# Performance work log

Hardware: AMD Instinct MI355X
Metric: run time of the kernel (lower is better)

## Reference

```python
import jax, jax.numpy as jnp
import numpy as np

N = 8192
IN_F = 512
OUT_F = 512
ALPHA = 0.2  # leaky relu slope


def setup_inputs() -> dict:
    key = jax.random.key(0)
    k1, k2, k3, k4, k5 = jax.random.split(key, 5)
    inp = jax.random.normal(k1, (N, IN_F), dtype=jnp.float32)
    adj = jax.random.randint(k2, (N, N), 0, 2, dtype=jnp.int32)
    # linear1: [in, out] + bias
    W1 = jax.random.normal(k3, (IN_F, OUT_F), dtype=jnp.float32) * (1.0 / np.sqrt(IN_F))
    b1 = jnp.zeros((OUT_F,), dtype=jnp.float32)
    # linear2: maps 2*out -> 1; split into the two halves acting on h_i and h_j
    a = jax.random.normal(k4, (2 * OUT_F,), dtype=jnp.float32) * (1.0 / np.sqrt(2 * OUT_F))
    a1 = a[:OUT_F]
    a2 = a[OUT_F:]
    b2 = jnp.zeros((), dtype=jnp.float32)
    return {"inp": inp, "adj": adj, "W1": W1, "b1": b1, "a1": a1, "a2": a2, "b2": b2}


def reference(inp, adj, W1, b1, a1, a2, b2):
    h = inp @ W1 + b1  # [N, out]
    # linear2(cat(h_i, h_j)) == h_i@a1 + h_j@a2 + b2 -> avoids the N*N*2F tensor
    e = jax.nn.leaky_relu((h @ a1)[:, None] + (h @ a2)[None, :] + b2, ALPHA)  # [N, N]
    attention = jnp.where(adj > 0, e, jnp.float32(-1e12))
    attention = jax.nn.softmax(attention, axis=1)
    h_prime = attention @ h  # [N, out]
    return jax.nn.elu(h_prime)  # concat=True
```

## Files before the change

kernel.cpp:

```cpp
#include <hip/hip_runtime.h>
#include <hip/hip_bf16.h>
#include <stdint.h>

#define NR 8192
#define FD 512
#define BM 64
#define BKC 128

typedef __attribute__((ext_vector_type(8))) short s8v;
typedef __attribute__((ext_vector_type(4))) float f32x4;

static __device__ __forceinline__ short bf16_rtne(float x) {
    union { float f; uint32_t u; } v; v.f = x;
    uint32_t r = (v.u + 0x7FFFu + ((v.u >> 16) & 1u)) >> 16;
    return (short)r;
}
static __device__ __forceinline__ float bf16_to_f32(short s) {
    union { uint32_t u; float f; } v; v.u = ((uint32_t)(uint16_t)s) << 16;
    return v.f;
}

__global__ void k_prepack(const int* __restrict__ adj, uint32_t* __restrict__ bm) {
    int t = blockIdx.x * 256 + threadIdx.x;
    const int4* p = (const int4*)(adj + (size_t)t * 32);
    uint32_t word = 0;
#pragma unroll
    for (int g = 0; g < 8; ++g) {
        int4 v = p[g];
        word |= (uint32_t)(v.x != 0) << (g * 4);
        word |= (uint32_t)(v.y != 0) << (g * 4 + 1);
        word |= (uint32_t)(v.z != 0) << (g * 4 + 2);
        word |= (uint32_t)(v.w != 0) << (g * 4 + 3);
    }
    bm[t] = word;
}

__global__ void k_convert(const float* __restrict__ in, short* __restrict__ out) {
    int i = blockIdx.x * blockDim.x + threadIdx.x;
    float4 v = ((const float4*)in)[i];
    short4 s;
    s.x = bf16_rtne(v.x); s.y = bf16_rtne(v.y);
    s.z = bf16_rtne(v.z); s.w = bf16_rtne(v.w);
    ((short4*)out)[i] = s;
}

__global__ void k_w1t(const float* __restrict__ W1, short* __restrict__ W1T) {
    int i = blockIdx.x * 256 + threadIdx.x;
    int k = i & 511, n = i >> 9;
    W1T[(size_t)n * 512 + k] = bf16_rtne(W1[(size_t)k * 512 + n]);
}

__launch_bounds__(256)
__global__ void k_gemm_h(const short* __restrict__ A,
                         const short* __restrict__ BT,
                         const float* __restrict__ b1,
                         short* __restrict__ H,
                         short* __restrict__ HT2)
{
    const int lane = threadIdx.x & 63;
    const int wn   = threadIdx.x >> 6;
    const int m    = lane & 15;
    const int q    = lane >> 4;
    const int r0   = blockIdx.x * 32;
    const int c0   = blockIdx.y * 128 + wn * 32;

    f32x4 acc[2][2] = {};
#pragma unroll 1
    for (int k0 = 0; k0 < 512; k0 += 32) {
        s8v a[2], b[2];
#pragma unroll
        for (int rt = 0; rt < 2; ++rt)
            a[rt] = *(const s8v*)(A + (size_t)(r0 + rt * 16 + m) * 512 + k0 + q * 8);
#pragma unroll
        for (int nt = 0; nt < 2; ++nt)
            b[nt] = *(const s8v*)(BT + (size_t)(c0 + nt * 16 + m) * 512 + k0 + q * 8);
#pragma unroll
        for (int rt = 0; rt < 2; ++rt)
#pragma unroll
            for (int nt = 0; nt < 2; ++nt)
                acc[rt][nt] = __builtin_amdgcn_mfma_f32_16x16x32_bf16(a[rt], b[nt], acc[rt][nt], 0, 0, 0);
    }
    float b1v[2];
#pragma unroll
    for (int nt = 0; nt < 2; ++nt) b1v[nt] = b1[c0 + nt * 16 + m];

#pragma unroll
    for (int rt = 0; rt < 2; ++rt)
#pragma unroll
        for (int nt = 0; nt < 2; ++nt) {
            int col = c0 + nt * 16 + m;
            short4 hp;
#pragma unroll
            for (int r = 0; r < 4; ++r) {
                int row = r0 + rt * 16 + q * 4 + r;
                short hv = bf16_rtne(acc[rt][nt][r] + b1v[nt]);
                H[(size_t)row * 512 + col] = hv;
                ((short*)&hp)[r] = hv;
            }
            *(short4*)(HT2 + (size_t)blockIdx.x * (512 * 32) + (size_t)col * 32 + rt * 16 + q * 4) = hp;
        }
}

__global__ void k_f1f2(const short* __restrict__ H, const float* __restrict__ a1,
                       const float* __restrict__ a2, const float* __restrict__ b2,
                       float* __restrict__ f1, float* __restrict__ f2s)
{
    const int lane = threadIdx.x & 63;
    const int row  = blockIdx.x * 4 + (threadIdx.x >> 6);
    s8v hv = *(const s8v*)(H + (size_t)row * 512 + lane * 8);
    float4 a1l = ((const float4*)(a1 + lane * 8))[0];
    float4 a1h = ((const float4*)(a1 + lane * 8))[1];
    float4 a2l = ((const float4*)(a2 + lane * 8))[0];
    float4 a2h = ((const float4*)(a2 + lane * 8))[1];
    float hf[8];
#pragma unroll
    for (int i = 0; i < 8; ++i) hf[i] = bf16_to_f32(hv[i]);
    float s1 = hf[0] * a1l.x + hf[1] * a1l.y + hf[2] * a1l.z + hf[3] * a1l.w
             + hf[4] * a1h.x + hf[5] * a1h.y + hf[6] * a1h.z + hf[7] * a1h.w;
    float s2 = hf[0] * a2l.x + hf[1] * a2l.y + hf[2] * a2l.z + hf[3] * a2l.w
             + hf[4] * a2h.x + hf[5] * a2h.y + hf[6] * a2h.z + hf[7] * a2h.w;
#pragma unroll
    for (int o = 32; o > 0; o >>= 1) {
        s1 += __shfl_xor(s1, o);
        s2 += __shfl_xor(s2, o);
    }
    if (lane == 0) {
        f1[row]  = s1;
        f2s[row] = s2 + b2[0];
    }
}

__launch_bounds__(512, 4)
__global__ void k_attn(const uint32_t* __restrict__ bm,
                       const short* __restrict__ HT2,
                       const float* __restrict__ f1,
                       const float* __restrict__ f2s,
                       float* __restrict__ nump,
                       float* __restrict__ denomp)
{
    __shared__ __align__(16) short wt[2][BM * BKC];

    const int t    = threadIdx.x;
    const int lane = t & 63;
    const int w    = t >> 6;
    const int m    = lane & 15;
    const int q    = lane >> 4;

    const int js   = blockIdx.x & 3;
    const int band = blockIdx.x >> 2;
    const int r0   = band * BM;
    const int jb0  = js * 2048;

    const int prow = t >> 3;
    const int jg   = t & 7;

    const float f1v = f1[r0 + prow];
    const uint16_t* bmp = (const uint16_t*)(bm + (size_t)(r0 + prow) * 256) + (jb0 >> 4) + jg;
    const float*    f2p = f2s + jb0 + jg * 16;

    f32x4 acc[4][4] = {};
    float dsum = 0.f;

    uint32_t bits = bmp[0];
    float4 fv[4];
#pragma unroll
    for (int g = 0; g < 4; ++g) fv[g] = ((const float4*)f2p)[g];

#pragma unroll 1
    for (int ch = 0; ch < 2048 / BKC; ++ch) {
        const int p = ch & 1;
        float wgt[16];
#pragma unroll
        for (int jj = 0; jj < 16; ++jj) {
            float s  = f1v + ((const float*)fv)[jj];
            float l  = fmaxf(s, 0.2f * s);
            float e  = __expf(l);
            float wv = ((bits >> jj) & 1u) ? e : 0.f;
            dsum += wv;
            wgt[jj] = wv;
        }
        s8v wv0, wv1;
#pragma unroll
        for (int jj = 0; jj < 8; ++jj) {
            wv0[jj] = bf16_rtne(wgt[jj]);
            wv1[jj] = bf16_rtne(wgt[8 + jj]);
        }
        const int sw = prow & 15;
        *(s8v*)&wt[p][prow * BKC + (((2 * jg) ^ sw) << 3)]     = wv0;
        *(s8v*)&wt[p][prow * BKC + (((2 * jg + 1) ^ sw) << 3)] = wv1;

        __syncthreads();

        const int chn = (ch + 1) & (2048 / BKC - 1);
        bits = bmp[chn * 8];
#pragma unroll
        for (int g = 0; g < 4; ++g) fv[g] = ((const float4*)(f2p + chn * BKC))[g];

#pragma unroll
        for (int kk = 0; kk < 4; ++kk) {
            const int jt = (jb0 + ch * BKC + kk * 32) >> 5;
            const short* hb = HT2 + (size_t)jt * 16384 + q * 8;
            s8v af[4];
#pragma unroll
            for (int i = 0; i < 4; ++i) {
                int row = i * 16 + m;
                af[i] = *(const s8v*)&wt[p][row * BKC + (((kk * 4 + q) ^ m) << 3)];
            }
#pragma unroll
            for (int nt = 0; nt < 4; ++nt) {
                s8v b = *(const s8v*)(hb + (size_t)(w * 64 + nt * 16 + m) * 32);
#pragma unroll
                for (int i = 0; i < 4; ++i)
                    acc[i][nt] = __builtin_amdgcn_mfma_f32_16x16x32_bf16(af[i], b, acc[i][nt], 0, 0, 0);
            }
        }
    }

    dsum += __shfl_xor(dsum, 1);
    dsum += __shfl_xor(dsum, 2);
    dsum += __shfl_xor(dsum, 4);
    if (jg == 0) denomp[(size_t)js * NR + r0 + prow] = dsum;

    float* np = nump + (size_t)js * NR * FD;
#pragma unroll
    for (int i = 0; i < 4; ++i)
#pragma unroll
        for (int nt = 0; nt < 4; ++nt)
#pragma unroll
            for (int r = 0; r < 4; ++r) {
                int row = r0 + i * 16 + q * 4 + r;
                int col = w * 64 + nt * 16 + m;
                np[(size_t)row * FD + col] = acc[i][nt][r];
            }
}

__global__ void k_combine(const float* __restrict__ nump,
                          const float* __restrict__ denomp,
                          float* __restrict__ out)
{
    size_t e = ((size_t)blockIdx.x * 256 + threadIdx.x) * 4;
    int row = (int)(e >> 9);
    float4 n0 = *(const float4*)(nump + e);
    float4 n1 = *(const float4*)(nump + (size_t)NR * FD + e);
    float4 n2 = *(const float4*)(nump + (size_t)2 * NR * FD + e);
    float4 n3 = *(const float4*)(nump + (size_t)3 * NR * FD + e);
    float d = denomp[row] + denomp[NR + row] + denomp[2 * NR + row] + denomp[3 * NR + row];
    float inv = 1.0f / d;
    float4 o;
    o.x = (n0.x + n1.x + n2.x + n3.x) * inv;
    o.y = (n0.y + n1.y + n2.y + n3.y) * inv;
    o.z = (n0.z + n1.z + n2.z + n3.z) * inv;
    o.w = (n0.w + n1.w + n2.w + n3.w) * inv;
    o.x = (o.x > 0.f) ? o.x : (__expf(o.x) - 1.f);
    o.y = (o.y > 0.f) ? o.y : (__expf(o.y) - 1.f);
    o.z = (o.z > 0.f) ? o.z : (__expf(o.z) - 1.f);
    o.w = (o.w > 0.f) ? o.w : (__expf(o.w) - 1.f);
    *(float4*)(out + e) = o;
}

extern "C" void kernel_launch(void* const* d_in, const int* in_sizes, int n_in,
                              void* d_out, int out_size, void* d_ws, size_t ws_size,
                              hipStream_t stream) {
    const float* inp = (const float*)d_in[0];
    const int*   adj = (const int*)d_in[1];
    const float* W1  = (const float*)d_in[2];
    const float* b1  = (const float*)d_in[3];
    const float* a1  = (const float*)d_in[4];
    const float* a2  = (const float*)d_in[5];
    const float* b2  = (const float*)d_in[6];
    float* out = (float*)d_out;

    short*    inp_bf = (short*)d_ws;
    short*    w1t    = inp_bf + (size_t)NR * FD;
    short*    h      = w1t + (size_t)FD * FD;
    short*    ht2    = h + (size_t)NR * FD;
    uint32_t* bmw    = (uint32_t*)(ht2 + (size_t)FD * NR);
    float*    f1     = (float*)(bmw + (size_t)NR * 256);
    float*    f2s    = f1 + NR;
    float*    nump   = f2s + NR;
    float*    denomp = nump + (size_t)4 * NR * FD;

    k_prepack<<<NR * 256 / 256, 256, 0, stream>>>(adj, bmw);
    k_convert<<<(NR * FD / 4) / 256, 256, 0, stream>>>(inp, inp_bf);
    k_w1t<<<(FD * FD) / 256, 256, 0, stream>>>(W1, w1t);
    dim3 g1(NR / 32, FD / 128);
    k_gemm_h<<<g1, 256, 0, stream>>>(inp_bf, w1t, b1, h, ht2);
    k_f1f2<<<NR / 4, 256, 0, stream>>>(h, a1, a2, b2, f1, f2s);
    k_attn<<<128 * 4, 512, 0, stream>>>(bmw, ht2, f1, f2s, nump, denomp);
    k_combine<<<(NR * FD / 4) / 256, 256, 0, stream>>>(nump, denomp, out);
}
```

Baseline: 565.9 us.

## Pipeline attention weight generation with MFMA, widen block, ballot-based adjacency packing

Restructures the attention kernel to use 1024-thread blocks with a 256-wide K chunk. The exp/mask weight computation for the next chunk now runs after the current chunk's MFMAs, so one barrier per iteration separates the LDS double buffer and the exp work can overlap matrix math. Each wave now covers 32 output columns instead of 64, which lowers accumulator register pressure but halves reuse of the A fragments. The adjacency prepack is rewritten to build 64-bit masks with wave ballots and fully coalesced int loads, changing the bit layout to match.

```diff
diff --git a/kernel.cpp b/kernel.cpp
--- a/kernel.cpp
+++ b/kernel.cpp
@@ -5,7 +5,7 @@
 #define NR 8192
 #define FD 512
 #define BM 64
-#define BKC 128
+#define BKC 256
 
 typedef __attribute__((ext_vector_type(8))) short s8v;
 typedef __attribute__((ext_vector_type(4))) float f32x4;
@@ -20,19 +20,25 @@
     return v.f;
 }
 
-__global__ void k_prepack(const int* __restrict__ adj, uint32_t* __restrict__ bm) {
-    int t = blockIdx.x * 256 + threadIdx.x;
-    const int4* p = (const int4*)(adj + (size_t)t * 32);
-    uint32_t word = 0;
+__global__ void k_prepack(const int* __restrict__ adj,
+                          unsigned long long* __restrict__ bm) {
+    const int lane = threadIdx.x & 63;
+    const int wv   = threadIdx.x >> 6;
+    const int gid  = blockIdx.x * 4 + wv;
+    const int row  = gid >> 2;
+    const int seg  = (gid & 3) * 2048;
+    const int* p   = adj + (size_t)row * NR + seg + lane;
+    unsigned long long* o = bm + (((size_t)row * NR + seg) >> 6);
 #pragma unroll
     for (int g = 0; g < 8; ++g) {
-        int4 v = p[g];
-        word |= (uint32_t)(v.x != 0) << (g * 4);
-        word |= (uint32_t)(v.y != 0) << (g * 4 + 1);
-        word |= (uint32_t)(v.z != 0) << (g * 4 + 2);
-        word |= (uint32_t)(v.w != 0) << (g * 4 + 3);
-    }
-    bm[t] = word;
+        unsigned long long b0 = __ballot(p[g * 256]       != 0);
+        unsigned long long b1 = __ballot(p[g * 256 + 64]  != 0);
+        unsigned long long b2 = __ballot(p[g * 256 + 128] != 0);
+        unsigned long long b3 = __ballot(p[g * 256 + 192] != 0);
+        unsigned long long vs = (lane == 0) ? b0 : (lane == 1) ? b1
+                              : (lane == 2) ? b2 : b3;
+        if (lane < 4) o[g * 4 + lane] = vs;
+    }
 }
 
 __global__ void k_convert(const float* __restrict__ in, short* __restrict__ out) {
@@ -130,7 +136,7 @@
     }
 }
 
-__launch_bounds__(512, 4)
+__launch_bounds__(1024, 4)
 __global__ void k_attn(const uint32_t* __restrict__ bm,
                        const short* __restrict__ HT2,
                        const float* __restrict__ f1,
@@ -151,85 +157,98 @@
     const int r0   = band * BM;
     const int jb0  = js * 2048;
 
-    const int prow = t >> 3;
-    const int jg   = t & 7;
+    const int prow = t >> 4;
+    const int jg   = t & 15;
 
     const float f1v = f1[r0 + prow];
-    const uint16_t* bmp = (const uint16_t*)(bm + (size_t)(r0 + prow) * 256) + (jb0 >> 4) + jg;
+    const uint16_t* bmp = (const uint16_t*)bm + (((size_t)(r0 + prow) * NR + jb0) >> 4) + jg;
     const float*    f2p = f2s + jb0 + jg * 16;
 
-    f32x4 acc[4][4] = {};
+    f32x4 acc[4][2] = {};
     float dsum = 0.f;
 
-    uint32_t bits = bmp[0];
+    uint32_t bits;
     float4 fv[4];
+
+#define GAT_PHASE1(PN)                                                        \
+    {                                                                         \
+        s8v wv0, wv1;                                                         \
+        _Pragma("unroll")                                                     \
+        for (int jj = 0; jj < 8; ++jj) {                                      \
+            float s_ = f1v + ((const float*)fv)[jj];                          \
+            float e_ = __expf(fmaxf(s_, 0.2f * s_));                          \
+            float x_ = ((bits >> jj) & 1u) ? e_ : 0.f;                        \
+            dsum += x_;                                                       \
+            wv0[jj] = bf16_rtne(x_);                                          \
+        }                                                                     \
+        _Pragma("unroll")                                                     \
+        for (int jj = 0; jj < 8; ++jj) {                                      \
+            float s_ = f1v + ((const float*)fv)[8 + jj];                      \
+            float e_ = __expf(fmaxf(s_, 0.2f * s_));                          \
+            float x_ = ((bits >> (8 + jj)) & 1u) ? e_ : 0.f;                  \
+            dsum += x_;                                                       \
+            wv1[jj] = bf16_rtne(x_);                                          \
+        }                                                                     \
+        const int sw = prow & 15;                                             \
+        *(s8v*)&wt[PN][prow * BKC + (((2 * jg) ^ sw) << 3)]     = wv0;        \
+        *(s8v*)&wt[PN][prow * BKC + (((2 * jg + 1) ^ sw) << 3)] = wv1;        \
+    }
+
+    bits = bmp[0];
 #pragma unroll
     for (int g = 0; g < 4; ++g) fv[g] = ((const float4*)f2p)[g];
+    GAT_PHASE1(0)
+    __syncthreads();
 
 #pragma unroll 1
     for (int ch = 0; ch < 2048 / BKC; ++ch) {
-        const int p = ch & 1;
-        float wgt[16];
-#pragma unroll
-        for (int jj = 0; jj < 16; ++jj) {
-            float s  = f1v + ((const float*)fv)[jj];
-            float l  = fmaxf(s, 0.2f * s);
-            float e  = __expf(l);
-            float wv = ((bits >> jj) & 1u) ? e : 0.f;
-            dsum += wv;
-            wgt[jj] = wv;
+        const int p   = ch & 1;
+        const int chn = ch + 1;
+        const bool more = (chn < 2048 / BKC);
+        if (more) {
+            bits = bmp[chn * 16];
+#pragma unroll
+            for (int g = 0; g < 4; ++g) fv[g] = ((const float4*)(f2p + chn * BKC))[g];
         }
-        s8v wv0, wv1;
-#pragma unroll
-        for (int jj = 0; jj < 8; ++jj) {
-            wv0[jj] = bf16_rtne(wgt[jj]);
-            wv1[jj] = bf16_rtne(wgt[8 + jj]);
-        }
-        const int sw = prow & 15;
-        *(s8v*)&wt[p][prow * BKC + (((2 * jg) ^ sw) << 3)]     = wv0;
-        *(s8v*)&wt[p][prow * BKC + (((2 * jg + 1) ^ sw) << 3)] = wv1;
-
-        __syncthreads();
-
-        const int chn = (ch + 1) & (2048 / BKC - 1);
-        bits = bmp[chn * 8];
-#pragma unroll
-        for (int g = 0; g < 4; ++g) fv[g] = ((const float4*)(f2p + chn * BKC))[g];
-
-#pragma unroll
-        for (int kk = 0; kk < 4; ++kk) {
+
+#pragma unroll
+        for (int kk = 0; kk < 8; ++kk) {
             const int jt = (jb0 + ch * BKC + kk * 32) >> 5;
             const short* hb = HT2 + (size_t)jt * 16384 + q * 8;
+            s8v b0 = *(const s8v*)(hb + (size_t)(w * 32 + m) * 32);
+            s8v b1 = *(const s8v*)(hb + (size_t)(w * 32 + 16 + m) * 32);
             s8v af[4];
 #pragma unroll
+            for (int i = 0; i < 4; ++i)
+                af[i] = *(const s8v*)&wt[p][(i * 16 + m) * BKC + (((kk * 4 + q) ^ m) << 3)];
+#pragma unroll
             for (int i = 0; i < 4; ++i) {
-                int row = i * 16 + m;
-                af[i] = *(const s8v*)&wt[p][row * BKC + (((kk * 4 + q) ^ m) << 3)];
-            }
-#pragma unroll
-            for (int nt = 0; nt < 4; ++nt) {
-                s8v b = *(const s8v*)(hb + (size_t)(w * 64 + nt * 16 + m) * 32);
-#pragma unroll
-                for (int i = 0; i < 4; ++i)
-                    acc[i][nt] = __builtin_amdgcn_mfma_f32_16x16x32_bf16(af[i], b, acc[i][nt], 0, 0, 0);
+                acc[i][0] = __builtin_amdgcn_mfma_f32_16x16x32_bf16(af[i], b0, acc[i][0], 0, 0, 0);
+                acc[i][1] = __builtin_amdgcn_mfma_f32_16x16x32_bf16(af[i], b1, acc[i][1], 0, 0, 0);
             }
         }
-    }
+
+        if (more) GAT_PHASE1(p ^ 1)
+
+        __syncthreads();
+    }
+#undef GAT_PHASE1
 
     dsum += __shfl_xor(dsum, 1);
     dsum += __shfl_xor(dsum, 2);
     dsum += __shfl_xor(dsum, 4);
+    dsum += __shfl_xor(dsum, 8);
     if (jg == 0) denomp[(size_t)js * NR + r0 + prow] = dsum;
 
     float* np = nump + (size_t)js * NR * FD;
 #pragma unroll
     for (int i = 0; i < 4; ++i)
 #pragma unroll
-        for (int nt = 0; nt < 4; ++nt)
+        for (int nt = 0; nt < 2; ++nt)
 #pragma unroll
             for (int r = 0; r < 4; ++r) {
                 int row = r0 + i * 16 + q * 4 + r;
-                int col = w * 64 + nt * 16 + m;
+                int col = w * 32 + nt * 16 + m;
                 np[(size_t)row * FD + col] = acc[i][nt][r];
             }
 }
@@ -280,12 +299,12 @@
     float*    nump   = f2s + NR;
     float*    denomp = nump + (size_t)4 * NR * FD;
 
-    k_prepack<<<NR * 256 / 256, 256, 0, stream>>>(adj, bmw);
+    k_prepack<<<NR, 256, 0, stream>>>(adj, (unsigned long long*)bmw);
     k_convert<<<(NR * FD / 4) / 256, 256, 0, stream>>>(inp, inp_bf);
     k_w1t<<<(FD * FD) / 256, 256, 0, stream>>>(W1, w1t);
     dim3 g1(NR / 32, FD / 128);
     k_gemm_h<<<g1, 256, 0, stream>>>(inp_bf, w1t, b1, h, ht2);
     k_f1f2<<<NR / 4, 256, 0, stream>>>(h, a1, a2, b2, f1, f2s);
-    k_attn<<<128 * 4, 512, 0, stream>>>(bmw, ht2, f1, f2s, nump, denomp);
+    k_attn<<<128 * 4, 1024, 0, stream>>>(bmw, ht2, f1, f2s, nump, denomp);
     k_combine<<<(NR * FD / 4) / 256, 256, 0, stream>>>(nump, denomp, out);
 }
```

After: 537.7 us. -5.0%, faster.
